# Kernel tuning notes

Measured on AMD Instinct MI355X. Metric: run time of the kernel, lower is better.

## Reference

```python
import jax, jax.numpy as jnp
import numpy as np

H = 4096          # hidden_size
NH = 32           # num_attention_heads
NKV = 2           # multi_query_group_num (kv heads)
HD = 128          # kv_channels / head_dim
RD = 64           # rotary_dim = head_dim * rotary_percent(0.5)
T = 2048          # total tokens (single prefill sequence)
EPS = 1e-5        # layernorm_epsilon
ROPE_BASE = 10000.0


def setup_inputs() -> dict:
    key = jax.random.key(0)
    k0, k1, k2, k3 = jax.random.split(key, 4)
    qkv_out = (NH + 2 * NKV) * HD  # 4608
    return {
        "positions": jnp.arange(T, dtype=jnp.int32),
        "hidden_states": jax.random.normal(k0, (T, H), jnp.float32),
        "w_qkv": jax.random.normal(k1, (qkv_out, H), jnp.float32) * 0.02,
        "b_qkv": jax.random.normal(k2, (qkv_out,), jnp.float32) * 0.02,
        "w_dense": jax.random.normal(k3, (H, NH * HD), jnp.float32) * 0.02,
        "q_ln_w": jnp.ones((HD,), jnp.float32),
        "k_ln_w": jnp.ones((HD,), jnp.float32),
    }


def _rmsnorm(x, w):
    # per-head RMSNorm over head_dim
    return x * jax.lax.rsqrt(jnp.mean(x * x, axis=-1, keepdims=True) + EPS) * w


def _rope(x, positions):
    # partial rotary (first RD dims), interleaved GPT-J style (is_neox_style=False)
    inv_freq = 1.0 / (ROPE_BASE ** (jnp.arange(0, RD, 2, dtype=jnp.float32) / RD))
    ang = positions.astype(jnp.float32)[:, None] * inv_freq      # [T, RD//2]
    cos = jnp.cos(ang)[:, None, :]                               # [T, 1, RD//2]
    sin = jnp.sin(ang)[:, None, :]
    x_rot, x_pass = x[..., :RD], x[..., RD:]
    x1 = x_rot[..., 0::2]
    x2 = x_rot[..., 1::2]
    r1 = x1 * cos - x2 * sin
    r2 = x2 * cos + x1 * sin
    x_rot = jnp.stack([r1, r2], axis=-1).reshape(x.shape[:-1] + (RD,))
    return jnp.concatenate([x_rot, x_pass], axis=-1)


def reference(positions, hidden_states, w_qkv, b_qkv, w_dense, q_ln_w, k_ln_w):
    qkv = hidden_states @ w_qkv.T + b_qkv                        # [T, 4608]
    q_size, kv_size = NH * HD, NKV * HD
    q = qkv[:, :q_size].reshape(T, NH, HD)
    k = qkv[:, q_size:q_size + kv_size].reshape(T, NKV, HD)
    v = qkv[:, q_size + kv_size:].reshape(T, NKV, HD)
    # optional qk layernorm (RMSNorm since config.rmsnorm)
    q = _rmsnorm(q, q_ln_w)
    k = _rmsnorm(k, k_ln_w)
    # rotary embedding
    q = _rope(q, positions)
    k = _rope(k, positions)
    # GQA: expand kv heads to query heads
    group = NH // NKV
    k_exp = jnp.repeat(k, group, axis=1)                         # [T, NH, HD]
    v_exp = jnp.repeat(v, group, axis=1)
    scale = HD ** -0.5
    scores = jnp.einsum("thd,shd->hts", q, k_exp) * scale        # [NH, T, T]
    causal = jnp.tril(jnp.ones((T, T), dtype=bool))
    scores = jnp.where(causal[None, :, :], scores, jnp.finfo(scores.dtype).min)
    attn = jax.nn.softmax(scores, axis=-1)
    out = jnp.einsum("hts,shd->thd", attn, v_exp).reshape(T, NH * HD)
    return out @ w_dense.T                                       # [T, H]
```

## Files before the change

### kernel.cpp

```cpp
#include <hip/hip_runtime.h>
#include <cstdint>
#include <cstddef>

typedef short short4v __attribute__((ext_vector_type(4)));
typedef short short8v __attribute__((ext_vector_type(8)));
typedef float f32x4   __attribute__((ext_vector_type(4)));

#define T_LEN  2048
#define HDIM   4096
#define NHEADS 32
#define HEADD  128
#define QKVN   4608

static __device__ __forceinline__ short f2bf(float f) {
  __bf16 h = (__bf16)f;
  return __builtin_bit_cast(short, h);
}

static __device__ __forceinline__ void gload_lds16(const void* g, void* l) {
  __builtin_amdgcn_global_load_lds((const __attribute__((address_space(1))) void*)g,
                                   (__attribute__((address_space(3))) void*)l,
                                   16, 0, 0);
}

__global__ void cast_f32_to_bf16(const float* __restrict__ in, short* __restrict__ out, int n4) {
  int idx = blockIdx.x * blockDim.x + threadIdx.x;
  int stride = gridDim.x * blockDim.x;
  const float4* in4 = (const float4*)in;
  short4v* out4 = (short4v*)out;
  for (int i = idx; i < n4; i += stride) {
    float4 v = in4[i];
    short4v o;
    o[0] = f2bf(v.x); o[1] = f2bf(v.y); o[2] = f2bf(v.z); o[3] = f2bf(v.w);
    out4[i] = o;
  }
}

__global__ __launch_bounds__(256, 2) void gemm_bt(
    const short* __restrict__ A,
    const short* __restrict__ B,
    const float* __restrict__ bias,
    float* __restrict__ Cout,
    int M, int N, int K)
{
  __shared__ short sA[128 * 32];
  __shared__ short sB[128 * 32];
  const int tid  = threadIdx.x;
  const int lane = tid & 63;
  const int wv   = tid >> 6;
  const int wr   = wv >> 1;
  const int wc   = wv & 1;
  const int bn0  = blockIdx.x * 128;
  const int bm0  = blockIdx.y * 128;

  const int row0 = tid >> 2;
  const int kc0  = (tid & 3) * 8;
  const int row1 = row0 + 64;
  short* lA0 = sA + wv * 64 * 8;
  short* lA1 = sA + (256 + wv * 64) * 8;
  short* lB0 = sB + wv * 64 * 8;
  short* lB1 = sB + (256 + wv * 64) * 8;
  const short* gA0 = A + (size_t)(bm0 + row0) * K + kc0;
  const short* gA1 = A + (size_t)(bm0 + row1) * K + kc0;
  const short* gB0 = B + (size_t)(bn0 + row0) * K + kc0;
  const short* gB1 = B + (size_t)(bn0 + row1) * K + kc0;

  const int fr = lane & 15;
  const int fk = (lane >> 4) * 8;

  f32x4 zero = {0.f, 0.f, 0.f, 0.f};
  f32x4 acc[4][4];
#pragma unroll
  for (int m = 0; m < 4; m++)
#pragma unroll
    for (int n = 0; n < 4; n++) acc[m][n] = zero;

  for (int kt = 0; kt < K; kt += 32) {
    gload_lds16(gA0 + kt, lA0);
    gload_lds16(gA1 + kt, lA1);
    gload_lds16(gB0 + kt, lB0);
    gload_lds16(gB1 + kt, lB1);
    __syncthreads();
    short8v af[4], bfr[4];
#pragma unroll
    for (int m = 0; m < 4; m++)
      af[m] = *(const short8v*)(sA + (wr * 64 + m * 16 + fr) * 32 + fk);
#pragma unroll
    for (int n = 0; n < 4; n++)
      bfr[n] = *(const short8v*)(sB + (wc * 64 + n * 16 + fr) * 32 + fk);
#pragma unroll
    for (int m = 0; m < 4; m++)
#pragma unroll
      for (int n = 0; n < 4; n++)
        acc[m][n] = __builtin_amdgcn_mfma_f32_16x16x32_bf16(af[m], bfr[n], acc[m][n], 0, 0, 0);
    __syncthreads();
  }

  const int rg = (lane >> 4) * 4;
#pragma unroll
  for (int m = 0; m < 4; m++) {
#pragma unroll
    for (int n = 0; n < 4; n++) {
      const int gcol = bn0 + wc * 64 + n * 16 + fr;
      const float bv = bias ? bias[gcol] : 0.0f;
#pragma unroll
      for (int j = 0; j < 4; j++) {
        const int grow = bm0 + wr * 64 + m * 16 + rg + j;
        Cout[(size_t)grow * N + gcol] = acc[m][n][j] + bv;
      }
    }
  }
}

__global__ __launch_bounds__(64) void qkv_post_kernel(
    const float* __restrict__ qkvf,
    const int*   __restrict__ positions,
    const float* __restrict__ q_ln,
    const float* __restrict__ k_ln,
    short* __restrict__ Qb,
    short* __restrict__ Kb,
    short* __restrict__ Vt)
{
  const int t = blockIdx.x;
  const int h = blockIdx.y;
  const int lane = threadIdx.x;
  const float2 x2 = ((const float2*)(qkvf + (size_t)t * QKVN + h * HEADD))[lane];
  float x = x2.x, y = x2.y;

  if (h >= 34) {
    const int hv = h - 34;
    short* dst = Vt + ((size_t)hv * HEADD + 2 * lane) * T_LEN + t;
    dst[0]     = f2bf(x);
    dst[T_LEN] = f2bf(y);
    return;
  }

  float ss = x * x + y * y;
#pragma unroll
  for (int d = 32; d > 0; d >>= 1) ss += __shfl_xor(ss, d);
  const float r = rsqrtf(ss * (1.0f / 128.0f) + 1e-5f);
  const float* lnw = (h < 32) ? q_ln : k_ln;
  x = x * r * lnw[2 * lane];
  y = y * r * lnw[2 * lane + 1];

  if (lane < 32) {
    const float pos = (float)positions[t];
    const float ang = pos * powf(10000.0f, -(float)lane * (1.0f / 32.0f));
    const float c = cosf(ang), s = sinf(ang);
    const float r1 = x * c - y * s;
    const float r2 = y * c + x * s;
    x = r1; y = r2;
  }

  short* dst = (h < 32) ? (Qb + ((size_t)h * T_LEN + t) * HEADD + 2 * lane)
                        : (Kb + ((size_t)(h - 32) * T_LEN + t) * HEADD + 2 * lane);
  dst[0] = f2bf(x);
  dst[1] = f2bf(y);
}

__global__ __launch_bounds__(256, 2) void attn_kernel(
    const short* __restrict__ Qb,
    const short* __restrict__ Kb,
    const short* __restrict__ Vt,
    short* __restrict__ attn_out)
{
  __shared__ short Ks[2][64 * 128];
  __shared__ short Vs[2][128 * 64];
  __shared__ short pbuf[4][32 * 64];
  const int blk  = gridDim.x - 1 - blockIdx.x;
  const int h    = blockIdx.y;
  const int hkv  = h >> 4;
  const int tid  = threadIdx.x;
  const int lane = tid & 63;
  const int wv   = tid >> 6;
  const int B0   = blk * 128;
  const int qrow0 = B0 + wv * 32;
  const int fr = lane & 15;
  const int fk = (lane >> 4) * 8;
  const int fkb = (lane >> 4) << 4;
  const int rg = (lane >> 4) * 4;
  const int swz = (fr & 7) << 4;

  const short* Kh = Kb + (size_t)hkv * T_LEN * HEADD;
  const short* Vh = Vt + (size_t)hkv * HEADD * T_LEN;

  short8v qf[2][4];
#pragma unroll
  for (int g = 0; g < 2; g++) {
    const short* Qrow = Qb + ((size_t)h * T_LEN + qrow0 + g * 16 + fr) * HEADD + fk;
#pragma unroll
    for (int d0 = 0; d0 < 4; d0++) qf[g][d0] = *(const short8v*)(Qrow + d0 * 32);
  }

  float mrow[2][4], lrow[2][4];
#pragma unroll
  for (int g = 0; g < 2; g++)
#pragma unroll
    for (int j = 0; j < 4; j++) { mrow[g][j] = -1e30f; lrow[g][j] = 0.f; }
  f32x4 zero = {0.f, 0.f, 0.f, 0.f};
  f32x4 o[2][8];
#pragma unroll
  for (int g = 0; g < 2; g++)
#pragma unroll
    for (int d = 0; d < 8; d++) o[g][d] = zero;

  char* pb = (char*)&pbuf[wv][0];
  const float scale = 0.08838834764831845f;
  const int nt = 2 * blk + 2;

  auto STAGE = [&](int b, int t) {
    const int s0 = t * 64;
#pragma unroll
    for (int i = 0; i < 4; i++) {
      const int c    = i * 256 + tid;
      const int row  = c >> 4;
      const int colb = (c & 15) << 4;
      const int scol = (colb ^ ((row & 7) << 4)) >> 1;
      gload_lds16(Kh + (size_t)(s0 + row) * HEADD + scol,
                  (char*)&Ks[b][0] + (size_t)(i * 256 + wv * 64) * 16);
    }
#pragma unroll
    for (int i = 0; i < 4; i++) {
      const int c    = i * 256 + tid;
      const int row  = c >> 3;
      const int colb = (c & 7) << 4;
      const int scol = (colb ^ ((row & 7) << 4)) >> 1;
      gload_lds16(Vh + (size_t)row * T_LEN + s0 + scol,
                  (char*)&Vs[b][0] + (size_t)(i * 256 + wv * 64) * 16);
    }
  };

  int cur = 0;
  STAGE(0, 0);
  __syncthreads();

  for (int t = 0; t < nt; ++t) {
    if (t + 1 < nt) STAGE(cur ^ 1, t + 1);
    const int s0 = t * 64;
    const char* KsB = (const char*)&Ks[cur][0];
    const char* VsB = (const char*)&Vs[cur][0];

    float scv[2][4][4];
#pragma unroll
    for (int sub = 0; sub < 4; sub++) {
      const char* Kbase = KsB + (sub * 16 + fr) * 256;
      f32x4 a0 = zero, a1 = zero;
#pragma unroll
      for (int d0 = 0; d0 < 4; d0++) {
        short8v kf = *(const short8v*)(Kbase + ((d0 * 64 + fkb) ^ swz));
        a0 = __builtin_amdgcn_mfma_f32_16x16x32_bf16(qf[0][d0], kf, a0, 0, 0, 0);
        a1 = __builtin_amdgcn_mfma_f32_16x16x32_bf16(qf[1][d0], kf, a1, 0, 0, 0);
      }
#pragma unroll
      for (int j = 0; j < 4; j++) {
        scv[0][sub][j] = a0[j] * scale;
        scv[1][sub][j] = a1[j] * scale;
      }
    }
    if (t >= nt - 2) {
#pragma unroll
      for (int g = 0; g < 2; g++)
#pragma unroll
        for (int sub = 0; sub < 4; sub++) {
          const int colp = s0 + sub * 16 + fr;
#pragma unroll
          for (int j = 0; j < 4; j++)
            if (colp > qrow0 + g * 16 + rg + j) scv[g][sub][j] = -1e30f;
        }
    }
    float pmax[2][4];
#pragma unroll
    for (int g = 0; g < 2; g++)
#pragma unroll
      for (int j = 0; j < 4; j++)
        pmax[g][j] = fmaxf(fmaxf(scv[g][0][j], scv[g][1][j]),
                           fmaxf(scv[g][2][j], scv[g][3][j]));
    float growth = -1e30f;
#pragma unroll
    for (int g = 0; g < 2; g++)
#pragma unroll
      for (int j = 0; j < 4; j++) growth = fmaxf(growth, pmax[g][j] - mrow[g][j]);
    if (!__all(growth <= 8.0f)) {
#pragma unroll
      for (int g = 0; g < 2; g++)
#pragma unroll
        for (int j = 0; j < 4; j++) {
          float mx = pmax[g][j];
#pragma unroll
          for (int d = 1; d < 16; d <<= 1) mx = fmaxf(mx, __shfl_xor(mx, d));
          const float mn = fmaxf(mrow[g][j], mx);
          const float c  = __expf(mrow[g][j] - mn);
          mrow[g][j] = mn;
          lrow[g][j] *= c;
#pragma unroll
          for (int df = 0; df < 8; df++) o[g][df][j] *= c;
        }
    }
#pragma unroll
    for (int g = 0; g < 2; g++)
#pragma unroll
      for (int j = 0; j < 4; j++) {
        const int prow = g * 16 + rg + j;
        char* prb = pb + prow * 128;
        const int rswz = ((rg + j) & 7) << 4;
        float ps = 0.f;
#pragma unroll
        for (int sub = 0; sub < 4; sub++) {
          const float p = __expf(scv[g][sub][j] - mrow[g][j]);
          ps += p;
          *(short*)(prb + ((((sub * 16 + fr) << 1)) ^ rswz)) = f2bf(p);
        }
        lrow[g][j] += ps;
      }
    asm volatile("" ::: "memory");
    short8v pf[2][2];
#pragma unroll
    for (int g = 0; g < 2; g++)
#pragma unroll
      for (int ks = 0; ks < 2; ks++)
        pf[g][ks] = *(const short8v*)(pb + (g * 16 + fr) * 128 + ((ks * 64 + fkb) ^ swz));
#pragma unroll
    for (int df = 0; df < 8; df++) {
      const char* Vbase = VsB + (df * 16 + fr) * 128;
      short8v vf0 = *(const short8v*)(Vbase + ((0 + fkb) ^ swz));
      short8v vf1 = *(const short8v*)(Vbase + ((64 + fkb) ^ swz));
      o[0][df] = __builtin_amdgcn_mfma_f32_16x16x32_bf16(pf[0][0], vf0, o[0][df], 0, 0, 0);
      o[0][df] = __builtin_amdgcn_mfma_f32_16x16x32_bf16(pf[0][1], vf1, o[0][df], 0, 0, 0);
      o[1][df] = __builtin_amdgcn_mfma_f32_16x16x32_bf16(pf[1][0], vf0, o[1][df], 0, 0, 0);
      o[1][df] = __builtin_amdgcn_mfma_f32_16x16x32_bf16(pf[1][1], vf1, o[1][df], 0, 0, 0);
    }
    __syncthreads();
    cur ^= 1;
  }

#pragma unroll
  for (int g = 0; g < 2; g++)
#pragma unroll
    for (int j = 0; j < 4; j++) {
#pragma unroll
      for (int d = 1; d < 16; d <<= 1) lrow[g][j] += __shfl_xor(lrow[g][j], d);
    }
#pragma unroll
  for (int g = 0; g < 2; g++)
#pragma unroll
    for (int df = 0; df < 8; df++)
#pragma unroll
      for (int j = 0; j < 4; j++) {
        const float v = o[g][df][j] / lrow[g][j];
        attn_out[(size_t)(qrow0 + g * 16 + rg + j) * HDIM + h * HEADD + df * 16 + fr] = f2bf(v);
      }
}

extern "C" void kernel_launch(void* const* d_in, const int* in_sizes, int n_in,
                              void* d_out, int out_size, void* d_ws, size_t ws_size,
                              hipStream_t stream) {
  (void)out_size; (void)ws_size;
  int ip = 0, ih = 1, iwq = 2, ib = 3, iwd = 4, il0 = 5, il1 = 6;
  if (n_in == 7) {
    int p = -1, hh = -1, wq = -1, b = -1, wd = -1, l0 = -1, l1 = -1, ok = 1;
    for (int i = 0; i < 7; i++) {
      switch (in_sizes[i]) {
        case 2048:     p  = i; break;
        case 8388608:  hh = i; break;
        case 18874368: wq = i; break;
        case 4608:     b  = i; break;
        case 16777216: wd = i; break;
        case 128:      if (l0 < 0) l0 = i; else l1 = i; break;
        default:       ok = 0; break;
      }
    }
    if (ok && p >= 0 && hh >= 0 && wq >= 0 && b >= 0 && wd >= 0 && l0 >= 0 && l1 >= 0) {
      ip = p; ih = hh; iwq = wq; ib = b; iwd = wd; il0 = l0; il1 = l1;
    }
  }

  const int*   positions = (const int*)d_in[ip];
  const float* hidden    = (const float*)d_in[ih];
  const float* w_qkv     = (const float*)d_in[iwq];
  const float* b_qkv     = (const float*)d_in[ib];
  const float* w_dense   = (const float*)d_in[iwd];
  const float* q_ln      = (const float*)d_in[il0];
  const float* k_ln      = (const float*)d_in[il1];

  char* ws = (char*)d_ws;
  short* Ahs   = (short*)(ws + 0);
  short* Qb    = (short*)(ws + 0);
  short* Wqkv  = (short*)(ws + (size_t)16777216);
  short* Kb    = (short*)(ws + (size_t)16777216);
  short* Vt    = (short*)(ws + (size_t)17825792);
  short* Wd    = (short*)(ws + (size_t)18874368);
  float* qkvf  = (float*)(ws + (size_t)54525952);
  short* attnb = (short*)(ws + (size_t)54525952);

  cast_f32_to_bf16<<<dim3(1024), dim3(256), 0, stream>>>(hidden, Ahs, (T_LEN * HDIM) / 4);
  cast_f32_to_bf16<<<dim3(2048), dim3(256), 0, stream>>>(w_qkv, Wqkv, (QKVN * HDIM) / 4);
  gemm_bt<<<dim3(QKVN / 128, T_LEN / 128), dim3(256), 0, stream>>>(
      Ahs, Wqkv, b_qkv, qkvf, T_LEN, QKVN, HDIM);
  qkv_post_kernel<<<dim3(T_LEN, 36), dim3(64), 0, stream>>>(
      qkvf, positions, q_ln, k_ln, Qb, Kb, Vt);
  cast_f32_to_bf16<<<dim3(2048), dim3(256), 0, stream>>>(w_dense, Wd, (HDIM * HDIM) / 4);
  attn_kernel<<<dim3(16, NHEADS), dim3(256), 0, stream>>>(Qb, Kb, Vt, attnb);
  gemm_bt<<<dim3(HDIM / 128, T_LEN / 128), dim3(256), 0, stream>>>(
      attnb, Wd, nullptr, (float*)d_out, T_LEN, HDIM, HDIM);
}
```

Measured before the change: 353.2 us.

## Double-buffer GEMM LDS tiles with K=64 steps and XOR swizzle

The bf16 GEMM kernel now uses two LDS buffers so the global-to-LDS load of the next K tile overlaps MFMA work on the current one. The K step doubles to 64, which halves the number of barriers. An XOR swizzle on LDS column offsets is meant to cut bank conflicts on the fragment reads. LDS use grows fourfold to 64 KB per block, which may lower occupancy under launch_bounds(256,2). Correctness relies on the single barrier per iteration being enough to order the async LDS writes against the reads.

```diff
diff --git a/kernel.cpp b/kernel.cpp
--- a/kernel.cpp
+++ b/kernel.cpp
@@ -43,8 +43,8 @@
     float* __restrict__ Cout,
     int M, int N, int K)
 {
-  __shared__ short sA[128 * 32];
-  __shared__ short sB[128 * 32];
+  __shared__ short sA[2][128 * 64];
+  __shared__ short sB[2][128 * 64];
   const int tid  = threadIdx.x;
   const int lane = tid & 63;
   const int wv   = tid >> 6;
@@ -53,20 +53,13 @@
   const int bn0  = blockIdx.x * 128;
   const int bm0  = blockIdx.y * 128;
 
-  const int row0 = tid >> 2;
-  const int kc0  = (tid & 3) * 8;
-  const int row1 = row0 + 64;
-  short* lA0 = sA + wv * 64 * 8;
-  short* lA1 = sA + (256 + wv * 64) * 8;
-  short* lB0 = sB + wv * 64 * 8;
-  short* lB1 = sB + (256 + wv * 64) * 8;
-  const short* gA0 = A + (size_t)(bm0 + row0) * K + kc0;
-  const short* gA1 = A + (size_t)(bm0 + row1) * K + kc0;
-  const short* gB0 = B + (size_t)(bn0 + row0) * K + kc0;
-  const short* gB1 = B + (size_t)(bn0 + row1) * K + kc0;
-
-  const int fr = lane & 15;
-  const int fk = (lane >> 4) * 8;
+  const int fr  = lane & 15;
+  const int fkb = (lane >> 4) << 4;
+  const int swz = (fr & 7) << 4;
+
+  const int c_row  = tid >> 3;
+  const int c_colb = (tid & 7) << 4;
+  const int c_scol = (c_colb ^ ((c_row & 7) << 4)) >> 1;
 
   f32x4 zero = {0.f, 0.f, 0.f, 0.f};
   f32x4 acc[4][4];
@@ -75,25 +68,50 @@
 #pragma unroll
     for (int n = 0; n < 4; n++) acc[m][n] = zero;
 
-  for (int kt = 0; kt < K; kt += 32) {
-    gload_lds16(gA0 + kt, lA0);
-    gload_lds16(gA1 + kt, lA1);
-    gload_lds16(gB0 + kt, lB0);
-    gload_lds16(gB1 + kt, lB1);
+  auto STAGE = [&](int b, int kt) {
+#pragma unroll
+    for (int i = 0; i < 4; i++) {
+      const int row = i * 32 + c_row;
+      gload_lds16(A + (size_t)(bm0 + row) * K + kt + c_scol,
+                  (char*)&sA[b][0] + (size_t)(i * 256 + wv * 64) * 16);
+    }
+#pragma unroll
+    for (int i = 0; i < 4; i++) {
+      const int row = i * 32 + c_row;
+      gload_lds16(B + (size_t)(bn0 + row) * K + kt + c_scol,
+                  (char*)&sB[b][0] + (size_t)(i * 256 + wv * 64) * 16);
+    }
+  };
+
+  int cur = 0;
+  STAGE(0, 0);
+  __syncthreads();
+
+  for (int kt = 0; kt < K; kt += 64) {
+    if (kt + 64 < K) STAGE(cur ^ 1, kt + 64);
+    const char* aB = (const char*)&sA[cur][0];
+    const char* bB = (const char*)&sB[cur][0];
+#pragma unroll
+    for (int ks = 0; ks < 2; ks++) {
+      short8v af[4], bfr[4];
+#pragma unroll
+      for (int m = 0; m < 4; m++) {
+        const int row = wr * 64 + m * 16 + fr;
+        af[m] = *(const short8v*)(aB + row * 128 + ((ks * 64 + fkb) ^ swz));
+      }
+#pragma unroll
+      for (int n = 0; n < 4; n++) {
+        const int row = wc * 64 + n * 16 + fr;
+        bfr[n] = *(const short8v*)(bB + row * 128 + ((ks * 64 + fkb) ^ swz));
+      }
+#pragma unroll
+      for (int m = 0; m < 4; m++)
+#pragma unroll
+        for (int n = 0; n < 4; n++)
+          acc[m][n] = __builtin_amdgcn_mfma_f32_16x16x32_bf16(af[m], bfr[n], acc[m][n], 0, 0, 0);
+    }
     __syncthreads();
-    short8v af[4], bfr[4];
-#pragma unroll
-    for (int m = 0; m < 4; m++)
-      af[m] = *(const short8v*)(sA + (wr * 64 + m * 16 + fr) * 32 + fk);
-#pragma unroll
-    for (int n = 0; n < 4; n++)
-      bfr[n] = *(const short8v*)(sB + (wc * 64 + n * 16 + fr) * 32 + fk);
-#pragma unroll
-    for (int m = 0; m < 4; m++)
-#pragma unroll
-      for (int n = 0; n < 4; n++)
-        acc[m][n] = __builtin_amdgcn_mfma_f32_16x16x32_bf16(af[m], bfr[n], acc[m][n], 0, 0, 0);
-    __syncthreads();
+    cur ^= 1;
   }
 
   const int rg = (lane >> 4) * 4;
```

Result: slower. 366.2 us (+3.7%).
